# Kernel tuning notes

Hardware: AMD Instinct MI355X
Metric: run time of the kernel (lower is better)

## Reference

```python
import jax, jax.numpy as jnp
import numpy as np

N = 8192
NHID = 256

def setup_inputs() -> dict:
    key = jax.random.key(0)
    k1, k2, k3 = jax.random.split(key, 3)
    x = jax.random.normal(k1, (N, NHID), dtype=jnp.float32)
    # dense (row-normalized-ish) adjacency; values in [0,1)
    adj = jax.random.uniform(k2, (N, N), dtype=jnp.float32) / N
    W = jax.random.normal(k3, (NHID, NHID), dtype=jnp.float32) * (1.0 / np.sqrt(NHID))
    b = jnp.zeros((NHID,), dtype=jnp.float32)
    return {"x": x, "adj": adj, "W": W, "b": b}

def reference(x, adj, W, b):
    # GCN layer: adj @ (x W) + b, then ReLU (dropout is identity at inference)
    support = x @ W + b            # [N, nhid]
    h = adj @ support              # [N, nhid]  (sparse-style aggregation, dense here)
    h = jax.nn.relu(h)
    # outer-product structure reconstruction
    return h @ h.T                 # [N, N]
```

## Files before the change

kernel.cpp:

```cpp
#include <hip/hip_runtime.h>
#include <hip/hip_bf16.h>
#include <stdint.h>

#define GLOBAL_AS __attribute__((address_space(1)))
#define LDS_AS    __attribute__((address_space(3)))

typedef __attribute__((ext_vector_type(8))) short          short8;
typedef __attribute__((ext_vector_type(4))) float          floatx4;
typedef __attribute__((ext_vector_type(4))) unsigned short ushort4v;

static __device__ __forceinline__ unsigned short f2bf_bits(float f) {
    union { float f; unsigned int u; } v; v.f = f;
    unsigned int r = v.u + 0x7FFFu + ((v.u >> 16) & 1u);
    return (unsigned short)(r >> 16);
}

static __device__ __forceinline__ floatx4 mfma16(short8 a, short8 b, floatx4 c) {
    return __builtin_amdgcn_mfma_f32_16x16x32_bf16(a, b, c, 0, 0, 0);
}

template<int BM, int BN, int BK, int WM, int WN, bool A_F32, bool B_F32, int EPI>
__global__ __launch_bounds__(256, 2)
void gemm_bt(const void* __restrict__ Ap, const void* __restrict__ Bp,
             const float* __restrict__ bias, void* __restrict__ Cp,
             int lda, int ldb, int ldc, int klen, long pstride)
{
    constexpr int NWM = BM / WM;
    constexpr int NWN = BN / WN;
    static_assert(NWM * NWN == 4, "4 waves per block");
    constexpr int FM = WM / 16;
    constexpr int FN = WN / 16;

    __shared__ __align__(16) unsigned short As[BM * BK];
    __shared__ __align__(16) unsigned short Bs[BN * BK];

    const int tid  = threadIdx.x;
    const int lane = tid & 63;
    const int wave = tid >> 6;
    const int wm   = (wave % NWM) * WM;
    const int wn   = (wave / NWM) * WN;
    const int quad = lane >> 4;
    const int l16  = lane & 15;
    const long m0 = (long)blockIdx.x * BM;
    const long n0 = (long)blockIdx.y * BN;
    const long k0 = (long)blockIdx.z * (long)klen;

    floatx4 acc[FM][FN];
#pragma unroll
    for (int i = 0; i < FM; ++i)
#pragma unroll
        for (int j = 0; j < FN; ++j) {
            floatx4 z = {0.f, 0.f, 0.f, 0.f};
            acc[i][j] = z;
        }

    for (int kk = 0; kk < klen; kk += BK) {
        {
            constexpr int CH = BM * BK / 8;
            if constexpr (A_F32) {
                const float* A = (const float*)Ap;
#pragma unroll
                for (int c0 = 0; c0 < CH; c0 += 256) {
                    int c   = c0 + tid;
                    int row = c / (BK / 8);
                    int col = (c % (BK / 8)) * 8;
                    const float* src = A + (m0 + row) * (long)lda + (k0 + kk + col);
                    floatx4 f0 = *(const floatx4*)(src);
                    floatx4 f1 = *(const floatx4*)(src + 4);
                    union { unsigned short u[8]; short8 v; } pk;
                    pk.u[0] = f2bf_bits(f0.x); pk.u[1] = f2bf_bits(f0.y);
                    pk.u[2] = f2bf_bits(f0.z); pk.u[3] = f2bf_bits(f0.w);
                    pk.u[4] = f2bf_bits(f1.x); pk.u[5] = f2bf_bits(f1.y);
                    pk.u[6] = f2bf_bits(f1.z); pk.u[7] = f2bf_bits(f1.w);
                    *(short8*)&As[c * 8] = pk.v;
                }
            } else {
                const unsigned short* A = (const unsigned short*)Ap;
#pragma unroll
                for (int c0 = 0; c0 < CH; c0 += 256) {
                    int c   = c0 + tid;
                    int row = c / (BK / 8);
                    int col = (c % (BK / 8)) * 8;
                    const unsigned short* src = A + (m0 + row) * (long)lda + (k0 + kk + col);
                    __builtin_amdgcn_global_load_lds((const GLOBAL_AS unsigned int*)src,
                                                     (LDS_AS unsigned int*)&As[c * 8],
                                                     16, 0, 0);
                }
            }
        }
        {
            constexpr int CH = BN * BK / 8;
            if constexpr (B_F32) {
                const float* B = (const float*)Bp;
#pragma unroll
                for (int c0 = 0; c0 < CH; c0 += 256) {
                    int c   = c0 + tid;
                    int row = c / (BK / 8);
                    int col = (c % (BK / 8)) * 8;
                    const float* src = B + (n0 + row) * (long)ldb + (k0 + kk + col);
                    floatx4 f0 = *(const floatx4*)(src);
                    floatx4 f1 = *(const floatx4*)(src + 4);
                    union { unsigned short u[8]; short8 v; } pk;
                    pk.u[0] = f2bf_bits(f0.x); pk.u[1] = f2bf_bits(f0.y);
                    pk.u[2] = f2bf_bits(f0.z); pk.u[3] = f2bf_bits(f0.w);
                    pk.u[4] = f2bf_bits(f1.x); pk.u[5] = f2bf_bits(f1.y);
                    pk.u[6] = f2bf_bits(f1.z); pk.u[7] = f2bf_bits(f1.w);
                    *(short8*)&Bs[c * 8] = pk.v;
                }
            } else {
                const unsigned short* B = (const unsigned short*)Bp;
#pragma unroll
                for (int c0 = 0; c0 < CH; c0 += 256) {
                    int c   = c0 + tid;
                    int row = c / (BK / 8);
                    int col = (c % (BK / 8)) * 8;
                    const unsigned short* src = B + (n0 + row) * (long)ldb + (k0 + kk + col);
                    __builtin_amdgcn_global_load_lds((const GLOBAL_AS unsigned int*)src,
                                                     (LDS_AS unsigned int*)&Bs[c * 8],
                                                     16, 0, 0);
                }
            }
        }
        __syncthreads();

#pragma unroll
        for (int ks = 0; ks < BK; ks += 32) {
            short8 af[FM], bfr[FN];
#pragma unroll
            for (int i = 0; i < FM; ++i)
                af[i] = *(const short8*)&As[(wm + i * 16 + l16) * BK + ks + quad * 8];
#pragma unroll
            for (int j = 0; j < FN; ++j)
                bfr[j] = *(const short8*)&Bs[(wn + j * 16 + l16) * BK + ks + quad * 8];
#pragma unroll
            for (int i = 0; i < FM; ++i)
#pragma unroll
                for (int j = 0; j < FN; ++j)
                    acc[i][j] = mfma16(af[i], bfr[j], acc[i][j]);
        }
        __syncthreads();
    }

#pragma unroll
    for (int i = 0; i < FM; ++i)
#pragma unroll
        for (int j = 0; j < FN; ++j)
#pragma unroll
            for (int v = 0; v < 4; ++v) {
                long r = m0 + wm + i * 16 + quad * 4 + v;
                long c = n0 + wn + j * 16 + l16;
                float val = acc[i][j][v];
                if constexpr (EPI == 0) {
                    val += bias[r];
                    ((unsigned short*)Cp)[r * (long)ldc + c] = f2bf_bits(val);
                } else if constexpr (EPI == 2) {
                    ((float*)Cp)[r * (long)ldc + c] = val;
                } else {
                    ((float*)Cp)[(long)blockIdx.z * pstride + r * (long)ldc + c] = val;
                }
            }
}

__global__ void transpose_w_kernel(const float* __restrict__ W, unsigned short* __restrict__ Wt)
{
    int idx = blockIdx.x * 256 + threadIdx.x;
    int n = idx >> 8;
    int k = idx & 255;
    Wt[n * 256 + k] = f2bf_bits(W[k * 256 + n]);
}

__global__ void reduce_relu_kernel(const float* __restrict__ p0, const float* __restrict__ p1,
                                   unsigned short* __restrict__ h)
{
    int i = (blockIdx.x * 256 + threadIdx.x) * 4;
    floatx4 a = *(const floatx4*)(p0 + i);
    floatx4 b = *(const floatx4*)(p1 + i);
    ushort4v o;
    o.x = f2bf_bits(fmaxf(a.x + b.x, 0.f));
    o.y = f2bf_bits(fmaxf(a.y + b.y, 0.f));
    o.z = f2bf_bits(fmaxf(a.z + b.z, 0.f));
    o.w = f2bf_bits(fmaxf(a.w + b.w, 0.f));
    *(ushort4v*)&h[i] = o;
}

extern "C" void kernel_launch(void* const* d_in, const int* in_sizes, int n_in,
                              void* d_out, int out_size, void* d_ws, size_t ws_size,
                              hipStream_t stream)
{
    const float* x   = (const float*)d_in[0];
    const float* adj = (const float*)d_in[1];
    const float* W   = (const float*)d_in[2];
    const float* b   = (const float*)d_in[3];
    float* out = (float*)d_out;

    char* ws = (char*)d_ws;
    unsigned short* Wt   = (unsigned short*)(ws);
    unsigned short* supT = (unsigned short*)(ws + 131072);
    unsigned short* h    = (unsigned short*)(ws + 4325376);
    float*          parts= (float*)         (ws + 8519680);
    const long PSTRIDE = 8192L * 256L;

    transpose_w_kernel<<<256, 256, 0, stream>>>(W, Wt);

    gemm_bt<32, 256, 64, 32, 64, false, true, 0>
        <<<dim3(8, 32, 1), 256, 0, stream>>>(Wt, x, b, supT, 256, 256, 8192, 256, 0);

    gemm_bt<32, 256, 64, 32, 64, true, false, 3>
        <<<dim3(256, 1, 2), 256, 0, stream>>>(adj, supT, nullptr, parts,
                                              8192, 8192, 256, 4096, PSTRIDE);

    reduce_relu_kernel<<<2048, 256, 0, stream>>>(parts, parts + PSTRIDE, h);

    gemm_bt<128, 128, 64, 64, 64, false, false, 2>
        <<<dim3(64, 64, 1), 256, 0, stream>>>(h, h, nullptr, out, 256, 256, 8192, 256, 0);
}
```

Baseline: 556.9 us.

## Exploit symmetry of h·hᵀ and retile adjacency GEMM with 4-way K split

Replaces the final h@h.T GEMM with a kernel that computes only lower-triangular 128x128 tiles and writes each off-diagonal tile twice, once transposed. This halves the MFMA work and the operand loads for the largest GEMM. The transposed stores are scattered across rows and may coalesce poorly. When the workspace is large enough, it also pre-casts x to bf16 and runs the adjacency GEMM with 64-row tiles and a 4-way K split, reducing four partial buffers.

```diff
diff --git a/kernel.cpp b/kernel.cpp
--- a/kernel.cpp
+++ b/kernel.cpp
@@ -161,6 +161,107 @@
             }
 }
 
+template<int BM, int BN, int BK, int WM, int WN>
+__global__ __launch_bounds__(256, 2)
+void gemm_sym(const unsigned short* __restrict__ A, float* __restrict__ C,
+              int ld, int ldc, int klen)
+{
+    constexpr int NWM = BM / WM;
+    constexpr int NWN = BN / WN;
+    static_assert(NWM * NWN == 4, "4 waves per block");
+    constexpr int FM = WM / 16;
+    constexpr int FN = WN / 16;
+
+    __shared__ __align__(16) unsigned short As[BM * BK];
+    __shared__ __align__(16) unsigned short Bs[BN * BK];
+
+    const int kblk = blockIdx.x;
+    int bi = (int)((sqrtf(8.f * (float)kblk + 1.f) - 1.f) * 0.5f);
+    while ((bi + 1) * (bi + 2) / 2 <= kblk) ++bi;
+    while (bi * (bi + 1) / 2 > kblk) --bi;
+    const int bj = kblk - bi * (bi + 1) / 2;
+
+    const long m0 = (long)bi * BM;
+    const long n0 = (long)bj * BN;
+
+    const int tid  = threadIdx.x;
+    const int lane = tid & 63;
+    const int wave = tid >> 6;
+    const int wm   = (wave % NWM) * WM;
+    const int wn   = (wave / NWM) * WN;
+    const int quad = lane >> 4;
+    const int l16  = lane & 15;
+
+    floatx4 acc[FM][FN];
+#pragma unroll
+    for (int i = 0; i < FM; ++i)
+#pragma unroll
+        for (int j = 0; j < FN; ++j) {
+            floatx4 z = {0.f, 0.f, 0.f, 0.f};
+            acc[i][j] = z;
+        }
+
+    for (int kk = 0; kk < klen; kk += BK) {
+        {
+            constexpr int CH = BM * BK / 8;
+#pragma unroll
+            for (int c0 = 0; c0 < CH; c0 += 256) {
+                int c   = c0 + tid;
+                int row = c / (BK / 8);
+                int col = (c % (BK / 8)) * 8;
+                const unsigned short* src = A + (m0 + row) * (long)ld + (kk + col);
+                __builtin_amdgcn_global_load_lds((const GLOBAL_AS unsigned int*)src,
+                                                 (LDS_AS unsigned int*)&As[c * 8],
+                                                 16, 0, 0);
+            }
+        }
+        {
+            constexpr int CH = BN * BK / 8;
+#pragma unroll
+            for (int c0 = 0; c0 < CH; c0 += 256) {
+                int c   = c0 + tid;
+                int row = c / (BK / 8);
+                int col = (c % (BK / 8)) * 8;
+                const unsigned short* src = A + (n0 + row) * (long)ld + (kk + col);
+                __builtin_amdgcn_global_load_lds((const GLOBAL_AS unsigned int*)src,
+                                                 (LDS_AS unsigned int*)&Bs[c * 8],
+                                                 16, 0, 0);
+            }
+        }
+        __syncthreads();
+
+#pragma unroll
+        for (int ks = 0; ks < BK; ks += 32) {
+            short8 af[FM], bfr[FN];
+#pragma unroll
+            for (int i = 0; i < FM; ++i)
+                af[i] = *(const short8*)&As[(wm + i * 16 + l16) * BK + ks + quad * 8];
+#pragma unroll
+            for (int j = 0; j < FN; ++j)
+                bfr[j] = *(const short8*)&Bs[(wn + j * 16 + l16) * BK + ks + quad * 8];
+#pragma unroll
+            for (int i = 0; i < FM; ++i)
+#pragma unroll
+                for (int j = 0; j < FN; ++j)
+                    acc[i][j] = mfma16(af[i], bfr[j], acc[i][j]);
+        }
+        __syncthreads();
+    }
+
+#pragma unroll
+    for (int i = 0; i < FM; ++i)
+#pragma unroll
+        for (int j = 0; j < FN; ++j) {
+            const long r0 = m0 + wm + i * 16 + quad * 4;
+            const long c  = n0 + wn + j * 16 + l16;
+#pragma unroll
+            for (int v = 0; v < 4; ++v)
+                C[(r0 + v) * (long)ldc + c] = acc[i][j][v];
+            if (bi != bj)
+                *(floatx4*)&C[c * (long)ldc + r0] = acc[i][j];
+        }
+}
+
 __global__ void transpose_w_kernel(const float* __restrict__ W, unsigned short* __restrict__ Wt)
 {
     int idx = blockIdx.x * 256 + threadIdx.x;
@@ -169,17 +270,33 @@
     Wt[n * 256 + k] = f2bf_bits(W[k * 256 + n]);
 }
 
-__global__ void reduce_relu_kernel(const float* __restrict__ p0, const float* __restrict__ p1,
+__global__ void cast_x_kernel(const float* __restrict__ x, unsigned short* __restrict__ xbf)
+{
+    int i = (blockIdx.x * 256 + threadIdx.x) * 8;
+    floatx4 a = *(const floatx4*)(x + i);
+    floatx4 b = *(const floatx4*)(x + i + 4);
+    union { unsigned short u[8]; short8 v; } pk;
+    pk.u[0] = f2bf_bits(a.x); pk.u[1] = f2bf_bits(a.y);
+    pk.u[2] = f2bf_bits(a.z); pk.u[3] = f2bf_bits(a.w);
+    pk.u[4] = f2bf_bits(b.x); pk.u[5] = f2bf_bits(b.y);
+    pk.u[6] = f2bf_bits(b.z); pk.u[7] = f2bf_bits(b.w);
+    *(short8*)&xbf[i] = pk.v;
+}
+
+__global__ void reduce_relu_kernel(const float* __restrict__ parts, long pstride, int nparts,
                                    unsigned short* __restrict__ h)
 {
     int i = (blockIdx.x * 256 + threadIdx.x) * 4;
-    floatx4 a = *(const floatx4*)(p0 + i);
-    floatx4 b = *(const floatx4*)(p1 + i);
+    floatx4 s = *(const floatx4*)(parts + i);
+    for (int p = 1; p < nparts; ++p) {
+        floatx4 t = *(const floatx4*)(parts + (long)p * pstride + i);
+        s.x += t.x; s.y += t.y; s.z += t.z; s.w += t.w;
+    }
     ushort4v o;
-    o.x = f2bf_bits(fmaxf(a.x + b.x, 0.f));
-    o.y = f2bf_bits(fmaxf(a.y + b.y, 0.f));
-    o.z = f2bf_bits(fmaxf(a.z + b.z, 0.f));
-    o.w = f2bf_bits(fmaxf(a.w + b.w, 0.f));
+    o.x = f2bf_bits(fmaxf(s.x, 0.f));
+    o.y = f2bf_bits(fmaxf(s.y, 0.f));
+    o.z = f2bf_bits(fmaxf(s.z, 0.f));
+    o.w = f2bf_bits(fmaxf(s.w, 0.f));
     *(ushort4v*)&h[i] = o;
 }
 
@@ -194,23 +311,50 @@
     float* out = (float*)d_out;
 
     char* ws = (char*)d_ws;
-    unsigned short* Wt   = (unsigned short*)(ws);
-    unsigned short* supT = (unsigned short*)(ws + 131072);
-    unsigned short* h    = (unsigned short*)(ws + 4325376);
-    float*          parts= (float*)         (ws + 8519680);
     const long PSTRIDE = 8192L * 256L;
 
-    transpose_w_kernel<<<256, 256, 0, stream>>>(W, Wt);
-
-    gemm_bt<32, 256, 64, 32, 64, false, true, 0>
-        <<<dim3(8, 32, 1), 256, 0, stream>>>(Wt, x, b, supT, 256, 256, 8192, 256, 0);
-
-    gemm_bt<32, 256, 64, 32, 64, true, false, 3>
-        <<<dim3(256, 1, 2), 256, 0, stream>>>(adj, supT, nullptr, parts,
-                                              8192, 8192, 256, 4096, PSTRIDE);
-
-    reduce_relu_kernel<<<2048, 256, 0, stream>>>(parts, parts + PSTRIDE, h);
-
-    gemm_bt<128, 128, 64, 64, 64, false, false, 2>
-        <<<dim3(64, 64, 1), 256, 0, stream>>>(h, h, nullptr, out, 256, 256, 8192, 256, 0);
-}
+    const size_t BIG_NEED = 12713984u + 4u * 8388608u;
+    const bool big = ws_size >= BIG_NEED;
+
+    if (big) {
+        unsigned short* Wt   = (unsigned short*)(ws);
+        unsigned short* xbf  = (unsigned short*)(ws + 131072);
+        unsigned short* supT = (unsigned short*)(ws + 4325376);
+        unsigned short* h    = (unsigned short*)(ws + 8519680);
+        float*          parts= (float*)         (ws + 12713984);
+
+        transpose_w_kernel<<<256, 256, 0, stream>>>(W, Wt);
+        cast_x_kernel<<<1024, 256, 0, stream>>>(x, xbf);
+
+        gemm_bt<32, 256, 64, 32, 64, false, false, 0>
+            <<<dim3(8, 32, 1), 256, 0, stream>>>(Wt, xbf, b, supT, 256, 256, 8192, 256, 0);
+
+        gemm_bt<64, 256, 64, 64, 64, true, false, 3>
+            <<<dim3(128, 1, 4), 256, 0, stream>>>(adj, supT, nullptr, parts,
+                                                  8192, 8192, 256, 2048, PSTRIDE);
+
+        reduce_relu_kernel<<<2048, 256, 0, stream>>>(parts, PSTRIDE, 4, h);
+
+        gemm_sym<128, 128, 64, 64, 64>
+            <<<dim3(2080, 1, 1), 256, 0, stream>>>(h, out, 256, 8192, 256);
+    } else {
+        unsigned short* Wt   = (unsigned short*)(ws);
+        unsigned short* supT = (unsigned short*)(ws + 131072);
+        unsigned short* h    = (unsigned short*)(ws + 4325376);
+        float*          parts= (float*)         (ws + 8519680);
+
+        transpose_w_kernel<<<256, 256, 0, stream>>>(W, Wt);
+
+        gemm_bt<32, 256, 64, 32, 64, false, true, 0>
+            <<<dim3(8, 32, 1), 256, 0, stream>>>(Wt, x, b, supT, 256, 256, 8192, 256, 0);
+
+        gemm_bt<32, 256, 64, 32, 64, true, false, 3>
+            <<<dim3(256, 1, 2), 256, 0, stream>>>(adj, supT, nullptr, parts,
+                                                  8192, 8192, 256, 4096, PSTRIDE);
+
+        reduce_relu_kernel<<<2048, 256, 0, stream>>>(parts, PSTRIDE, 2, h);
+
+        gemm_sym<128, 128, 64, 64, 64>
+            <<<dim3(2080, 1, 1), 256, 0, stream>>>(h, out, 256, 8192, 256);
+    }
+}
```

Result: no change. 548.3 us (-1.6%).
